# Optimization experiments

Measured on AMD Instinct MI355X. Metric: run time of the kernel, lower is better.

The kernel has to match this reference:

```python
import jax, jax.numpy as jnp
import numpy as np

LATENT, HID, STYLE, D, B = 16, 512, 64, 8, 16384


def _lin(key, fan_in, fan_out):
    kw, kb = jax.random.split(key)
    s = 1.0 / np.sqrt(fan_in)
    return (jax.random.uniform(kw, (fan_in, fan_out), jnp.float32, -s, s),
            jax.random.uniform(kb, (fan_out,), jnp.float32, -s, s))


def setup_inputs() -> dict:
    key = jax.random.key(0)
    ks = jax.random.split(key, 12)
    x = jax.random.normal(ks[0], (B, LATENT), jnp.float32)
    y = jax.random.randint(ks[1], (B,), 0, D)
    # shared MLP: latent->512, 512->512 x3, each followed by ReLU
    W0, b0 = _lin(ks[2], LATENT, HID)
    W1, b1 = _lin(ks[3], HID, HID)
    W2, b2 = _lin(ks[4], HID, HID)
    W3, b3 = _lin(ks[5], HID, HID)
    # unshared per-domain 4-layer MLPs, stacked along domain axis d
    def _stack(k, fi, fo):
        Ws, bs = [], []
        for kk in jax.random.split(k, D):
            w, b = _lin(kk, fi, fo)
            Ws.append(w); bs.append(b)
        return jnp.stack(Ws), jnp.stack(bs)
    U0, c0 = _stack(ks[6], HID, HID)
    U1, c1 = _stack(ks[7], HID, HID)
    U2, c2 = _stack(ks[8], HID, HID)
    U3, c3 = _stack(ks[9], HID, STYLE)
    return {"x": x, "y": y,
            "W0": W0, "b0": b0, "W1": W1, "b1": b1,
            "W2": W2, "b2": b2, "W3": W3, "b3": b3,
            "U0": U0, "c0": c0, "U1": U1, "c1": c1,
            "U2": U2, "c2": c2, "U3": U3, "c3": c3}


def reference(x, y, W0, b0, W1, b1, W2, b2, W3, b3,
              U0, c0, U1, c1, U2, c2, U3, c3):
    # shared trunk
    h = jax.nn.relu(x @ W0 + b0)
    h = jax.nn.relu(h @ W1 + b1)
    h = jax.nn.relu(h @ W2 + b2)
    h = jax.nn.relu(h @ W3 + b3)            # [B, HID]
    # run all D expert MLPs batched, then select per-sample by domain y
    g = jax.nn.relu(jnp.einsum('bi,dio->dbo', h, U0) + c0[:, None, :])
    g = jax.nn.relu(jnp.einsum('dbi,dio->dbo', g, U1) + c1[:, None, :])
    g = jax.nn.relu(jnp.einsum('dbi,dio->dbo', g, U2) + c2[:, None, :])
    g = jnp.einsum('dbi,dio->dbo', g, U3) + c3[:, None, :]   # [D, B, STYLE]
    out = g[y, jnp.arange(g.shape[1])]       # [B, STYLE]
    return out
```

## Files before the change

### kernel.cpp

```cpp
#include <hip/hip_runtime.h>

typedef _Float16 f16;
typedef _Float16 f16x4 __attribute__((ext_vector_type(4)));
typedef _Float16 f16x8 __attribute__((ext_vector_type(8)));
typedef float f32x4 __attribute__((ext_vector_type(4)));

#define B_TOT 16384
#define LAT_  16
#define STY_  64
#define ND_   8

#define ROWS 64
#define NTHR 1024
#define NBLK 256


__global__ void prep_k(const float* W0, f16* Wt0, const float* W1, f16* Wt1,
                       const float* W2, f16* Wt2, const float* W3, f16* Wt3,
                       const float* U0, f16* U0t, const float* U1, f16* U1t,
                       const float* U2, f16* U2t, const float* U3, f16* U3t) {
  int z = blockIdx.z;
  const float* src; f16* dst; int Kin, Nin, Kpad, NR;
  if (z == 0)      { src = W0; dst = Wt0; Kin = 16;  Nin = 512; Kpad = 32;  NR = 512; }
  else if (z == 1) { src = W1; dst = Wt1; Kin = 512; Nin = 512; Kpad = 512; NR = 512; }
  else if (z == 2) { src = W2; dst = Wt2; Kin = 512; Nin = 512; Kpad = 512; NR = 512; }
  else if (z == 3) { src = W3; dst = Wt3; Kin = 512; Nin = 512; Kpad = 512; NR = 512; }
  else if (z < 12) { int d = z - 4;  src = U0 + (long)d * 262144; dst = U0t + (long)d * 262144; Kin = 512; Nin = 512; Kpad = 512; NR = 512; }
  else if (z < 20) { int d = z - 12; src = U1 + (long)d * 262144; dst = U1t + (long)d * 262144; Kin = 512; Nin = 512; Kpad = 512; NR = 512; }
  else if (z < 28) { int d = z - 20; src = U2 + (long)d * 262144; dst = U2t + (long)d * 262144; Kin = 512; Nin = 512; Kpad = 512; NR = 512; }
  else             { int d = z - 28; src = U3 + (long)d * 32768;  dst = U3t + (long)d * 32768;  Kin = 512; Nin = 64;  Kpad = 512; NR = 64; }

  __shared__ float tile[32][33];
  int k0 = blockIdx.y * 32, n0 = blockIdx.x * 32;
  int tx = threadIdx.x, ty = threadIdx.y;
  #pragma unroll
  for (int i = 0; i < 32; i += 8) {
    int k = k0 + ty + i, n = n0 + tx;
    tile[ty + i][tx] = (k < Kin && n < Nin) ? src[(long)k * Nin + n] : 0.f;
  }
  __syncthreads();
  #pragma unroll
  for (int i = 0; i < 32; i += 8) {
    int n = n0 + ty + i, k = k0 + tx;
    if (n < NR && k < Kpad)
      dst[(long)(((k >> 5) * NR + n) << 5) | (k & 31)] = (f16)tile[tx][ty + i];
  }
}

#define NT_BUCKET 1024
#define RPT 16

__global__ __launch_bounds__(NT_BUCKET) void bucket_k(const int* __restrict__ y,
                                                      int* __restrict__ offsets,
                                                      int* __restrict__ perm) {
  __shared__ int hist[ND_][NT_BUCKET];
  __shared__ int totals[ND_];
  __shared__ int bases[ND_ + 1];
  int t = threadIdx.x;
  int base = t * RPT;

  #pragma unroll
  for (int d = 0; d < ND_; d++) hist[d][t] = 0;
  int yv[RPT];
  #pragma unroll
  for (int i = 0; i < RPT; i++) {
    yv[i] = y[base + i];
    hist[yv[i]][t]++;
  }
  __syncthreads();

  int wave = t >> 6, lane = t & 63;
  if (wave < ND_) {
    int d = wave;
    int carry = 0;
    for (int c = 0; c < NT_BUCKET; c += 64) {
      int v = hist[d][c + lane];
      int s = v;
      #pragma unroll
      for (int off = 1; off < 64; off <<= 1) {
        int u = __shfl_up(s, off, 64);
        if (lane >= off) s += u;
      }
      hist[d][c + lane] = carry + s - v;
      carry += __shfl(s, 63, 64);
    }
    if (lane == 0) totals[d] = carry;
  }
  __syncthreads();

  if (t == 0) {
    int s = 0;
    #pragma unroll
    for (int d = 0; d < ND_; d++) { bases[d] = s; offsets[d] = s; s += totals[d]; }
    bases[ND_] = s; offsets[ND_] = s;
  }
  __syncthreads();

  #pragma unroll
  for (int i = 0; i < RPT; i++) {
    int d = yv[i];
    int pos = bases[d] + hist[d][t];
    hist[d][t]++;
    perm[pos] = base + i;
  }
}

#define MFMA_(b, a, c) __builtin_amdgcn_mfma_f32_16x16x32_f16((b), (a), (c), 0, 0, 0)

template<int KT, bool FINAL>
__device__ __forceinline__ void do_layer(
    const f16* __restrict__ Wk, const float* __restrict__ bias,
    f16* __restrict__ act, int rlo, int rhi,
    const int* __restrict__ perm, int slot0, float* __restrict__ out, int t) {
  const int lane = t & 63, wid = t >> 6;
  const int lr = lane & 15, lg = lane >> 4;
  char* actb = (char*)act;

  __syncthreads();

  if (!FINAL) {
    const int wn = wid * 32;
    const f16* wp[2];
    #pragma unroll
    for (int n = 0; n < 2; n++)
      wp[n] = Wk + ((wn + n * 16 + lr) * 32 + lg * 8);
    const char* ab[4];
    #pragma unroll
    for (int m = 0; m < 4; m++)
      ab[m] = actb + m * 1024 + lg * 256 + lr * 16;

    f32x4 acc[4][2];
    #pragma unroll
    for (int m = 0; m < 4; m++) {
      acc[m][0] = f32x4{0.f, 0.f, 0.f, 0.f};
      acc[m][1] = f32x4{0.f, 0.f, 0.f, 0.f};
    }

    f16x8 bf[4][2], af[2][4];
    #pragma unroll
    for (int n = 0; n < 2; n++) bf[0][n] = *(const f16x8*)(wp[n]);
    if constexpr (KT > 1) {
      #pragma unroll
      for (int n = 0; n < 2; n++) bf[1][n] = *(const f16x8*)(wp[n] + 16384);
    }
    if constexpr (KT > 2) {
      #pragma unroll
      for (int n = 0; n < 2; n++) bf[2][n] = *(const f16x8*)(wp[n] + 2 * 16384);
    }
    #pragma unroll
    for (int m = 0; m < 4; m++) af[0][m] = *(const f16x8*)(ab[m]);

    #pragma unroll
    for (int kt = 0; kt < KT; kt++) {
      if (kt + 3 < KT) {
        #pragma unroll
        for (int n = 0; n < 2; n++)
          bf[(kt + 3) & 3][n] = *(const f16x8*)(wp[n] + (kt + 3) * 16384);
      }
      if (kt + 1 < KT) {
        #pragma unroll
        for (int m = 0; m < 4; m++)
          af[(kt + 1) & 1][m] = *(const f16x8*)(ab[m] + (kt + 1) * 4096);
      }
      #pragma unroll
      for (int m = 0; m < 4; m++)
        #pragma unroll
        for (int n = 0; n < 2; n++)
          acc[m][n] = MFMA_(bf[kt & 3][n], af[kt & 1][m], acc[m][n]);
    }

    __syncthreads();

    #pragma unroll
    for (int m = 0; m < 4; m++) {
      int r = m * 16 + lr;
      bool ok = (r >= rlo) && (r < rhi);
      #pragma unroll
      for (int n = 0; n < 2; n++) {
        f32x4 bb = *(const f32x4*)(bias + wn + n * 16 + lg * 4);
        f16x4 h;
        #pragma unroll
        for (int j = 0; j < 4; j++)
          h[j] = (f16)fmaxf(acc[m][n][j] + bb[j], 0.f);
        int byte = (wid * 4 + m) * 1024 + (n * 2 + (lg >> 1)) * 256
                 + lr * 16 + (lg & 1) * 8;
        if (ok)
          *(f16x4*)(actb + byte) = h;
      }
    }
  } else {
    const int mf = wid >> 2, nf = wid & 3;
    const f16* wp = Wk + ((nf * 16 + lr) * 32 + lg * 8);
    const char* abf = actb + mf * 1024 + lg * 256 + lr * 16;
    f32x4 a = f32x4{0.f, 0.f, 0.f, 0.f};
    f16x8 wbuf[4], abuf[2];
    wbuf[0] = *(const f16x8*)(wp);
    wbuf[1] = *(const f16x8*)(wp + 2048);
    wbuf[2] = *(const f16x8*)(wp + 2 * 2048);
    abuf[0] = *(const f16x8*)(abf);
    #pragma unroll
    for (int kt = 0; kt < 16; kt++) {
      if (kt + 3 < 16) wbuf[(kt + 3) & 3] = *(const f16x8*)(wp + (kt + 3) * 2048);
      if (kt + 1 < 16) abuf[(kt + 1) & 1] = *(const f16x8*)(abf + (kt + 1) * 4096);
      a = MFMA_(wbuf[kt & 3], abuf[kt & 1], a);
    }
    int r = mf * 16 + lr;
    if (r >= rlo && r < rhi) {
      int orig = perm[slot0 + r];
      int cn0 = nf * 16 + lg * 4;
      f32x4 bb = *(const f32x4*)(bias + cn0);
      f32x4 v;
      #pragma unroll
      for (int j = 0; j < 4; j++) v[j] = a[j] + bb[j];
      *(f32x4*)(out + (long)orig * STY_ + cn0) = v;
    }
  }
}

__global__ __launch_bounds__(NTHR, 4) void fused_k(
    const float* __restrict__ x,
    const f16* __restrict__ Wt0, const float* __restrict__ b0,
    const f16* __restrict__ Wt1, const float* __restrict__ b1,
    const f16* __restrict__ Wt2, const float* __restrict__ b2,
    const f16* __restrict__ Wt3, const float* __restrict__ b3,
    const f16* __restrict__ U0t, const float* __restrict__ c0,
    const f16* __restrict__ U1t, const float* __restrict__ c1,
    const f16* __restrict__ U2t, const float* __restrict__ c2,
    const f16* __restrict__ U3t, const float* __restrict__ c3,
    const int* __restrict__ offs, const int* __restrict__ perm,
    float* __restrict__ out) {
  __shared__ f16 act[16 * 64 * 32];

  int t = threadIdx.x;
  int wg = (blockIdx.x & 7) * (NBLK / 8) + (blockIdx.x >> 3);
  int slot0 = wg * ROWS;

  char* actb = (char*)act;
  #pragma unroll
  for (int i = 0; i < 2; i++) {
    int e = i * NTHR + t;
    int r = e >> 5, c = e & 31;
    int orig = perm[slot0 + r];
    f16 v = (c < LAT_) ? (f16)x[orig * LAT_ + c] : (f16)0.f;
    int byte = (r >> 4) * 1024 + ((c >> 3) & 3) * 256 + (r & 15) * 16 + (c & 7) * 2;
    *(f16*)(actb + byte) = v;
  }

  int d0 = 0, d1 = 0;
  #pragma unroll
  for (int d = 1; d < ND_; d++) {
    d0 += (slot0 >= offs[d]);
    d1 += (slot0 + ROWS - 1 >= offs[d]);
  }

  do_layer<1,  false>(Wt0, b0, act, 0, ROWS, perm, slot0, out, t);
  do_layer<16, false>(Wt1, b1, act, 0, ROWS, perm, slot0, out, t);
  do_layer<16, false>(Wt2, b2, act, 0, ROWS, perm, slot0, out, t);
  do_layer<16, false>(Wt3, b3, act, 0, ROWS, perm, slot0, out, t);

  #pragma unroll 1
  for (int d = d0; d <= d1; d++) {
    int rlo = (d == d0) ? 0 : (offs[d] - slot0);
    int rhi = (d == d1) ? ROWS : (offs[d + 1] - slot0);
    do_layer<16, false>(U0t + (long)d * 262144, c0 + d * 512,
                        act, rlo, rhi, perm, slot0, out, t);
  }
  #pragma unroll 1
  for (int d = d0; d <= d1; d++) {
    int rlo = (d == d0) ? 0 : (offs[d] - slot0);
    int rhi = (d == d1) ? ROWS : (offs[d + 1] - slot0);
    do_layer<16, false>(U1t + (long)d * 262144, c1 + d * 512,
                        act, rlo, rhi, perm, slot0, out, t);
  }
  #pragma unroll 1
  for (int d = d0; d <= d1; d++) {
    int rlo = (d == d0) ? 0 : (offs[d] - slot0);
    int rhi = (d == d1) ? ROWS : (offs[d + 1] - slot0);
    do_layer<16, false>(U2t + (long)d * 262144, c2 + d * 512,
                        act, rlo, rhi, perm, slot0, out, t);
  }
  #pragma unroll 1
  for (int d = d0; d <= d1; d++) {
    int rlo = (d == d0) ? 0 : (offs[d] - slot0);
    int rhi = (d == d1) ? ROWS : (offs[d + 1] - slot0);
    do_layer<16, true>(U3t + (long)d * 32768, c3 + d * 64,
                       act, rlo, rhi, perm, slot0, out, t);
  }
}


extern "C" void kernel_launch(void* const* d_in, const int* in_sizes, int n_in,
                              void* d_out, int out_size, void* d_ws, size_t ws_size,
                              hipStream_t stream) {
  const float* x  = (const float*)d_in[0];
  const int*   y  = (const int*)  d_in[1];
  const float* W0 = (const float*)d_in[2];
  const float* b0 = (const float*)d_in[3];
  const float* W1 = (const float*)d_in[4];
  const float* b1 = (const float*)d_in[5];
  const float* W2 = (const float*)d_in[6];
  const float* b2 = (const float*)d_in[7];
  const float* W3 = (const float*)d_in[8];
  const float* b3 = (const float*)d_in[9];
  const float* U0 = (const float*)d_in[10];
  const float* c0 = (const float*)d_in[11];
  const float* U1 = (const float*)d_in[12];
  const float* c1 = (const float*)d_in[13];
  const float* U2 = (const float*)d_in[14];
  const float* c2 = (const float*)d_in[15];
  const float* U3 = (const float*)d_in[16];
  const float* c3 = (const float*)d_in[17];
  float* out = (float*)d_out;

  char* p = (char*)d_ws;
  auto alloc = [&](size_t bytes) -> char* {
    char* r = p; p += (bytes + 255) & ~(size_t)255; return r;
  };
  f16* Wt0 = (f16*)alloc((size_t)512 * 32 * 2);
  f16* Wt1 = (f16*)alloc((size_t)512 * 512 * 2);
  f16* Wt2 = (f16*)alloc((size_t)512 * 512 * 2);
  f16* Wt3 = (f16*)alloc((size_t)512 * 512 * 2);
  f16* U0t = (f16*)alloc((size_t)ND_ * 512 * 512 * 2);
  f16* U1t = (f16*)alloc((size_t)ND_ * 512 * 512 * 2);
  f16* U2t = (f16*)alloc((size_t)ND_ * 512 * 512 * 2);
  f16* U3t = (f16*)alloc((size_t)ND_ * 16 * 64 * 32 * 2);
  int* offsets = (int*)alloc((ND_ + 1) * 4);
  int* perm    = (int*)alloc((size_t)B_TOT * 4);

  prep_k<<<dim3(16, 16, 36), dim3(32, 8), 0, stream>>>(W0, Wt0, W1, Wt1, W2, Wt2, W3, Wt3,
                                                       U0, U0t, U1, U1t, U2, U2t, U3, U3t);
  bucket_k<<<1, NT_BUCKET, 0, stream>>>(y, offsets, perm);
  fused_k<<<NBLK, NTHR, 0, stream>>>(x, Wt0, b0, Wt1, b1, Wt2, b2, Wt3, b3,
                                     U0t, c0, U1t, c1, U2t, c2, U3t, c3,
                                     offsets, perm, out);
}
```

Baseline: 113.9 us.

## Merge weight prep, bucketing and fused MLP into one cooperative kernel

```diff
diff --git a/kernel.cpp b/kernel.cpp
--- a/kernel.cpp
+++ b/kernel.cpp
@@ -1,4 +1,7 @@
 #include <hip/hip_runtime.h>
+#include <hip/hip_cooperative_groups.h>
+
+namespace cg = cooperative_groups;
 
 typedef _Float16 f16;
 typedef _Float16 f16x4 __attribute__((ext_vector_type(4)));
@@ -14,96 +17,8 @@
 #define NTHR 1024
 #define NBLK 256
 
-
-__global__ void prep_k(const float* W0, f16* Wt0, const float* W1, f16* Wt1,
-                       const float* W2, f16* Wt2, const float* W3, f16* Wt3,
-                       const float* U0, f16* U0t, const float* U1, f16* U1t,
-                       const float* U2, f16* U2t, const float* U3, f16* U3t) {
-  int z = blockIdx.z;
-  const float* src; f16* dst; int Kin, Nin, Kpad, NR;
-  if (z == 0)      { src = W0; dst = Wt0; Kin = 16;  Nin = 512; Kpad = 32;  NR = 512; }
-  else if (z == 1) { src = W1; dst = Wt1; Kin = 512; Nin = 512; Kpad = 512; NR = 512; }
-  else if (z == 2) { src = W2; dst = Wt2; Kin = 512; Nin = 512; Kpad = 512; NR = 512; }
-  else if (z == 3) { src = W3; dst = Wt3; Kin = 512; Nin = 512; Kpad = 512; NR = 512; }
-  else if (z < 12) { int d = z - 4;  src = U0 + (long)d * 262144; dst = U0t + (long)d * 262144; Kin = 512; Nin = 512; Kpad = 512; NR = 512; }
-  else if (z < 20) { int d = z - 12; src = U1 + (long)d * 262144; dst = U1t + (long)d * 262144; Kin = 512; Nin = 512; Kpad = 512; NR = 512; }
-  else if (z < 28) { int d = z - 20; src = U2 + (long)d * 262144; dst = U2t + (long)d * 262144; Kin = 512; Nin = 512; Kpad = 512; NR = 512; }
-  else             { int d = z - 28; src = U3 + (long)d * 32768;  dst = U3t + (long)d * 32768;  Kin = 512; Nin = 64;  Kpad = 512; NR = 64; }
-
-  __shared__ float tile[32][33];
-  int k0 = blockIdx.y * 32, n0 = blockIdx.x * 32;
-  int tx = threadIdx.x, ty = threadIdx.y;
-  #pragma unroll
-  for (int i = 0; i < 32; i += 8) {
-    int k = k0 + ty + i, n = n0 + tx;
-    tile[ty + i][tx] = (k < Kin && n < Nin) ? src[(long)k * Nin + n] : 0.f;
-  }
-  __syncthreads();
-  #pragma unroll
-  for (int i = 0; i < 32; i += 8) {
-    int n = n0 + ty + i, k = k0 + tx;
-    if (n < NR && k < Kpad)
-      dst[(long)(((k >> 5) * NR + n) << 5) | (k & 31)] = (f16)tile[tx][ty + i];
-  }
-}
-
-#define NT_BUCKET 1024
-#define RPT 16
-
-__global__ __launch_bounds__(NT_BUCKET) void bucket_k(const int* __restrict__ y,
-                                                      int* __restrict__ offsets,
-                                                      int* __restrict__ perm) {
-  __shared__ int hist[ND_][NT_BUCKET];
-  __shared__ int totals[ND_];
-  __shared__ int bases[ND_ + 1];
-  int t = threadIdx.x;
-  int base = t * RPT;
-
-  #pragma unroll
-  for (int d = 0; d < ND_; d++) hist[d][t] = 0;
-  int yv[RPT];
-  #pragma unroll
-  for (int i = 0; i < RPT; i++) {
-    yv[i] = y[base + i];
-    hist[yv[i]][t]++;
-  }
-  __syncthreads();
-
-  int wave = t >> 6, lane = t & 63;
-  if (wave < ND_) {
-    int d = wave;
-    int carry = 0;
-    for (int c = 0; c < NT_BUCKET; c += 64) {
-      int v = hist[d][c + lane];
-      int s = v;
-      #pragma unroll
-      for (int off = 1; off < 64; off <<= 1) {
-        int u = __shfl_up(s, off, 64);
-        if (lane >= off) s += u;
-      }
-      hist[d][c + lane] = carry + s - v;
-      carry += __shfl(s, 63, 64);
-    }
-    if (lane == 0) totals[d] = carry;
-  }
-  __syncthreads();
-
-  if (t == 0) {
-    int s = 0;
-    #pragma unroll
-    for (int d = 0; d < ND_; d++) { bases[d] = s; offsets[d] = s; s += totals[d]; }
-    bases[ND_] = s; offsets[ND_] = s;
-  }
-  __syncthreads();
-
-  #pragma unroll
-  for (int i = 0; i < RPT; i++) {
-    int d = yv[i];
-    int pos = bases[d] + hist[d][t];
-    hist[d][t]++;
-    perm[pos] = base + i;
-  }
-}
+#define NTILE 7184
+
 
 #define MFMA_(b, a, c) __builtin_amdgcn_mfma_f32_16x16x32_f16((b), (a), (c), 0, 0, 0)
 
@@ -118,7 +33,7 @@
 
   __syncthreads();
 
-  if (!FINAL) {
+  if constexpr (!FINAL) {
     const int wn = wid * 32;
     const f16* wp[2];
     #pragma unroll
@@ -217,25 +132,118 @@
   }
 }
 
-__global__ __launch_bounds__(NTHR, 4) void fused_k(
-    const float* __restrict__ x,
-    const f16* __restrict__ Wt0, const float* __restrict__ b0,
-    const f16* __restrict__ Wt1, const float* __restrict__ b1,
-    const f16* __restrict__ Wt2, const float* __restrict__ b2,
-    const f16* __restrict__ Wt3, const float* __restrict__ b3,
-    const f16* __restrict__ U0t, const float* __restrict__ c0,
-    const f16* __restrict__ U1t, const float* __restrict__ c1,
-    const f16* __restrict__ U2t, const float* __restrict__ c2,
-    const f16* __restrict__ U3t, const float* __restrict__ c3,
-    const int* __restrict__ offs, const int* __restrict__ perm,
+__global__ __launch_bounds__(NTHR, 4) void mega_k(
+    const float* __restrict__ x, const int* __restrict__ y,
+    const float* W0, const float* b0, const float* W1, const float* b1,
+    const float* W2, const float* b2, const float* W3, const float* b3,
+    const float* U0, const float* c0, const float* U1, const float* c1,
+    const float* U2, const float* c2, const float* U3, const float* c3,
+    f16* Wt0, f16* Wt1, f16* Wt2, f16* Wt3,
+    f16* U0t, f16* U1t, f16* U2t, f16* U3t,
+    int* __restrict__ offsets, int* __restrict__ perm,
     float* __restrict__ out) {
-  __shared__ f16 act[16 * 64 * 32];
+  __shared__ __align__(16) char smem[65536];
 
   int t = threadIdx.x;
-  int wg = (blockIdx.x & 7) * (NBLK / 8) + (blockIdx.x >> 3);
+  int bid = blockIdx.x;
+
+  if (bid < 255) {
+    float (*tile)[32][33] = (float (*)[32][33])smem;
+    int sub = t >> 8, tt = t & 255;
+    int tx = tt & 31, ty = tt >> 5;
+    for (int it = 0; it < 8; ++it) {
+      int g = (it * 255 + bid) * 4 + sub;
+      bool active = (g < NTILE);
+      int gg = active ? g : 0;
+      int z, nx, ky;
+      if (gg < 16)        { z = 0; nx = gg; ky = 0; }
+      else if (gg < 6928) { int r = gg - 16; z = 1 + (r >> 8); r &= 255; ky = r >> 4; nx = r & 15; }
+      else                { int r = gg - 6928; z = 28 + (r >> 5); r &= 31; nx = r >> 4; ky = r & 15; }
+      const float* src; f16* dst; int Kin, Nin, Kpad, NR;
+      if (z == 0)      { src = W0; dst = Wt0; Kin = 16;  Nin = 512; Kpad = 32;  NR = 512; }
+      else if (z == 1) { src = W1; dst = Wt1; Kin = 512; Nin = 512; Kpad = 512; NR = 512; }
+      else if (z == 2) { src = W2; dst = Wt2; Kin = 512; Nin = 512; Kpad = 512; NR = 512; }
+      else if (z == 3) { src = W3; dst = Wt3; Kin = 512; Nin = 512; Kpad = 512; NR = 512; }
+      else if (z < 12) { int d = z - 4;  src = U0 + (long)d * 262144; dst = U0t + (long)d * 262144; Kin = 512; Nin = 512; Kpad = 512; NR = 512; }
+      else if (z < 20) { int d = z - 12; src = U1 + (long)d * 262144; dst = U1t + (long)d * 262144; Kin = 512; Nin = 512; Kpad = 512; NR = 512; }
+      else if (z < 28) { int d = z - 20; src = U2 + (long)d * 262144; dst = U2t + (long)d * 262144; Kin = 512; Nin = 512; Kpad = 512; NR = 512; }
+      else             { int d = z - 28; src = U3 + (long)d * 32768;  dst = U3t + (long)d * 32768;  Kin = 512; Nin = 64;  Kpad = 512; NR = 64; }
+
+      int k0 = ky * 32, n0 = nx * 32;
+      #pragma unroll
+      for (int i = 0; i < 32; i += 8) {
+        int k = k0 + ty + i, n = n0 + tx;
+        tile[sub][ty + i][tx] =
+            (active && k < Kin && n < Nin) ? src[(long)k * Nin + n] : 0.f;
+      }
+      __syncthreads();
+      #pragma unroll
+      for (int i = 0; i < 32; i += 8) {
+        int n = n0 + ty + i, k = k0 + tx;
+        if (active && n < NR && k < Kpad)
+          dst[(long)(((k >> 5) * NR + n) << 5) | (k & 31)] = (f16)tile[sub][tx][ty + i];
+      }
+      __syncthreads();
+    }
+  } else {
+    int (*hist)[NTHR] = (int (*)[NTHR])smem;
+    __shared__ int totals[ND_];
+    __shared__ int bases[ND_];
+    #pragma unroll
+    for (int d = 0; d < ND_; d++) hist[d][t] = 0;
+    int base = t * 16;
+    int yv[16];
+    #pragma unroll
+    for (int i = 0; i < 16; i++) {
+      yv[i] = y[base + i];
+      hist[yv[i]][t]++;
+    }
+    __syncthreads();
+
+    int wave = t >> 6, lane = t & 63;
+    if (wave < ND_) {
+      int d = wave;
+      int carry = 0;
+      for (int c = 0; c < NTHR; c += 64) {
+        int v = hist[d][c + lane];
+        int s = v;
+        #pragma unroll
+        for (int off = 1; off < 64; off <<= 1) {
+          int u = __shfl_up(s, off, 64);
+          if (lane >= off) s += u;
+        }
+        hist[d][c + lane] = carry + s - v;
+        carry += __shfl(s, 63, 64);
+      }
+      if (lane == 0) totals[d] = carry;
+    }
+    __syncthreads();
+
+    if (t == 0) {
+      int s = 0;
+      #pragma unroll
+      for (int d = 0; d < ND_; d++) { bases[d] = s; offsets[d] = s; s += totals[d]; }
+      offsets[ND_] = s;
+    }
+    __syncthreads();
+
+    #pragma unroll
+    for (int i = 0; i < 16; i++) {
+      int d = yv[i];
+      int pos = bases[d] + hist[d][t];
+      hist[d][t]++;
+      perm[pos] = base + i;
+    }
+  }
+
+  cg::this_grid().sync();
+
+  f16* act = (f16*)smem;
+  char* actb = smem;
+
+  int wg = (bid & 7) * (NBLK / 8) + (bid >> 3);
   int slot0 = wg * ROWS;
 
-  char* actb = (char*)act;
   #pragma unroll
   for (int i = 0; i < 2; i++) {
     int e = i * NTHR + t;
@@ -249,8 +257,8 @@
   int d0 = 0, d1 = 0;
   #pragma unroll
   for (int d = 1; d < ND_; d++) {
-    d0 += (slot0 >= offs[d]);
-    d1 += (slot0 + ROWS - 1 >= offs[d]);
+    d0 += (slot0 >= offsets[d]);
+    d1 += (slot0 + ROWS - 1 >= offsets[d]);
   }
 
   do_layer<1,  false>(Wt0, b0, act, 0, ROWS, perm, slot0, out, t);
@@ -260,29 +268,29 @@
 
   #pragma unroll 1
   for (int d = d0; d <= d1; d++) {
-    int rlo = (d == d0) ? 0 : (offs[d] - slot0);
-    int rhi = (d == d1) ? ROWS : (offs[d + 1] - slot0);
+    int rlo = (d == d0) ? 0 : (offsets[d] - slot0);
+    int rhi = (d == d1) ? ROWS : (offsets[d + 1] - slot0);
     do_layer<16, false>(U0t + (long)d * 262144, c0 + d * 512,
                         act, rlo, rhi, perm, slot0, out, t);
   }
   #pragma unroll 1
   for (int d = d0; d <= d1; d++) {
-    int rlo = (d == d0) ? 0 : (offs[d] - slot0);
-    int rhi = (d == d1) ? ROWS : (offs[d + 1] - slot0);
+    int rlo = (d == d0) ? 0 : (offsets[d] - slot0);
+    int rhi = (d == d1) ? ROWS : (offsets[d + 1] - slot0);
     do_layer<16, false>(U1t + (long)d * 262144, c1 + d * 512,
                         act, rlo, rhi, perm, slot0, out, t);
   }
   #pragma unroll 1
   for (int d = d0; d <= d1; d++) {
-    int rlo = (d == d0) ? 0 : (offs[d] - slot0);
-    int rhi = (d == d1) ? ROWS : (offs[d + 1] - slot0);
+    int rlo = (d == d0) ? 0 : (offsets[d] - slot0);
+    int rhi = (d == d1) ? ROWS : (offsets[d + 1] - slot0);
     do_layer<16, false>(U2t + (long)d * 262144, c2 + d * 512,
                         act, rlo, rhi, perm, slot0, out, t);
   }
   #pragma unroll 1
   for (int d = d0; d <= d1; d++) {
-    int rlo = (d == d0) ? 0 : (offs[d] - slot0);
-    int rhi = (d == d1) ? ROWS : (offs[d + 1] - slot0);
+    int rlo = (d == d0) ? 0 : (offsets[d] - slot0);
+    int rhi = (d == d1) ? ROWS : (offsets[d + 1] - slot0);
     do_layer<16, true>(U3t + (long)d * 32768, c3 + d * 64,
                        act, rlo, rhi, perm, slot0, out, t);
   }
@@ -327,10 +335,16 @@
   int* offsets = (int*)alloc((ND_ + 1) * 4);
   int* perm    = (int*)alloc((size_t)B_TOT * 4);
 
-  prep_k<<<dim3(16, 16, 36), dim3(32, 8), 0, stream>>>(W0, Wt0, W1, Wt1, W2, Wt2, W3, Wt3,
-                                                       U0, U0t, U1, U1t, U2, U2t, U3, U3t);
-  bucket_k<<<1, NT_BUCKET, 0, stream>>>(y, offsets, perm);
-  fused_k<<<NBLK, NTHR, 0, stream>>>(x, Wt0, b0, Wt1, b1, Wt2, b2, Wt3, b3,
-                                     U0t, c0, U1t, c1, U2t, c2, U3t, c3,
-                                     offsets, perm, out);
+  void* args[] = {
+    (void*)&x, (void*)&y,
+    (void*)&W0, (void*)&b0, (void*)&W1, (void*)&b1,
+    (void*)&W2, (void*)&b2, (void*)&W3, (void*)&b3,
+    (void*)&U0, (void*)&c0, (void*)&U1, (void*)&c1,
+    (void*)&U2, (void*)&c2, (void*)&U3, (void*)&c3,
+    (void*)&Wt0, (void*)&Wt1, (void*)&Wt2, (void*)&Wt3,
+    (void*)&U0t, (void*)&U1t, (void*)&U2t, (void*)&U3t,
+    (void*)&offsets, (void*)&perm, (void*)&out
+  };
+  hipLaunchCooperativeKernel((const void*)mega_k, dim3(NBLK), dim3(NTHR),
+                             args, 0, stream);
 }
```

Result: slower. 142.7 us (+25.3%).

## Stage weight tiles into LDS via direct global-to-LDS loads with double buffering

Applied to the files above, without the earlier changes.

```diff
diff --git a/kernel.cpp b/kernel.cpp
--- a/kernel.cpp
+++ b/kernel.cpp
@@ -14,6 +14,12 @@
 #define NTHR 1024
 #define NBLK 256
 
+
+__device__ __forceinline__ void gload16(const f16* g, f16* l) {
+  __builtin_amdgcn_global_load_lds(
+      (const __attribute__((address_space(1))) unsigned int*)g,
+      (__attribute__((address_space(3))) unsigned int*)l, 16, 0, 0);
+}
 
 __global__ void prep_k(const float* W0, f16* Wt0, const float* W1, f16* Wt1,
                        const float* W2, f16* Wt2, const float* W3, f16* Wt3,
@@ -42,8 +48,11 @@
   #pragma unroll
   for (int i = 0; i < 32; i += 8) {
     int n = n0 + ty + i, k = k0 + tx;
-    if (n < NR && k < Kpad)
-      dst[(long)(((k >> 5) * NR + n) << 5) | (k & 31)] = (f16)tile[tx][ty + i];
+    if (n < NR && k < Kpad) {
+      long idx = (long)(k >> 5) * (NR * 32) + (n >> 4) * 512
+               + ((k >> 3) & 3) * 128 + (n & 15) * 8 + (k & 7);
+      dst[idx] = (f16)tile[tx][ty + i];
+    }
   }
 }
 
@@ -92,7 +101,7 @@
     int s = 0;
     #pragma unroll
     for (int d = 0; d < ND_; d++) { bases[d] = s; offsets[d] = s; s += totals[d]; }
-    bases[ND_] = s; offsets[ND_] = s;
+    offsets[ND_] = s;
   }
   __syncthreads();
 
@@ -110,20 +119,16 @@
 template<int KT, bool FINAL>
 __device__ __forceinline__ void do_layer(
     const f16* __restrict__ Wk, const float* __restrict__ bias,
-    f16* __restrict__ act, int rlo, int rhi,
+    f16* __restrict__ act, f16* __restrict__ wls,
+    int rlo, int rhi,
     const int* __restrict__ perm, int slot0, float* __restrict__ out, int t) {
   const int lane = t & 63, wid = t >> 6;
   const int lr = lane & 15, lg = lane >> 4;
   char* actb = (char*)act;
 
-  __syncthreads();
-
-  if (!FINAL) {
+  if constexpr (!FINAL) {
     const int wn = wid * 32;
-    const f16* wp[2];
-    #pragma unroll
-    for (int n = 0; n < 2; n++)
-      wp[n] = Wk + ((wn + n * 16 + lr) * 32 + lg * 8);
+    const f16* wsrc = Wk + wid * 512 + lane * 8;
     const char* ab[4];
     #pragma unroll
     for (int m = 0; m < 4; m++)
@@ -136,40 +141,32 @@
       acc[m][1] = f32x4{0.f, 0.f, 0.f, 0.f};
     }
 
-    f16x8 bf[4][2], af[2][4];
-    #pragma unroll
-    for (int n = 0; n < 2; n++) bf[0][n] = *(const f16x8*)(wp[n]);
-    if constexpr (KT > 1) {
-      #pragma unroll
-      for (int n = 0; n < 2; n++) bf[1][n] = *(const f16x8*)(wp[n] + 16384);
-    }
-    if constexpr (KT > 2) {
-      #pragma unroll
-      for (int n = 0; n < 2; n++) bf[2][n] = *(const f16x8*)(wp[n] + 2 * 16384);
-    }
-    #pragma unroll
-    for (int m = 0; m < 4; m++) af[0][m] = *(const f16x8*)(ab[m]);
+    gload16(wsrc, wls + wid * 512);
+    gload16(wsrc + 8192, wls + 8192 + wid * 512);
+    __syncthreads();
 
     #pragma unroll
     for (int kt = 0; kt < KT; kt++) {
-      if (kt + 3 < KT) {
-        #pragma unroll
-        for (int n = 0; n < 2; n++)
-          bf[(kt + 3) & 3][n] = *(const f16x8*)(wp[n] + (kt + 3) * 16384);
+      if (kt + 1 < KT) {
+        const f16* s = wsrc + (kt + 1) * 16384;
+        f16* d = wls + ((kt + 1) & 1) * 16384;
+        gload16(s, d + wid * 512);
+        gload16(s + 8192, d + 8192 + wid * 512);
       }
-      if (kt + 1 < KT) {
-        #pragma unroll
-        for (int m = 0; m < 4; m++)
-          af[(kt + 1) & 1][m] = *(const f16x8*)(ab[m] + (kt + 1) * 4096);
+      const f16* wb = wls + (kt & 1) * 16384;
+      f16x8 b0 = *(const f16x8*)(wb + (wid * 2 + 0) * 512 + lane * 8);
+      f16x8 b1 = *(const f16x8*)(wb + (wid * 2 + 1) * 512 + lane * 8);
+      f16x8 af[4];
+      #pragma unroll
+      for (int m = 0; m < 4; m++)
+        af[m] = *(const f16x8*)(ab[m] + kt * 4096);
+      #pragma unroll
+      for (int m = 0; m < 4; m++) {
+        acc[m][0] = MFMA_(b0, af[m], acc[m][0]);
+        acc[m][1] = MFMA_(b1, af[m], acc[m][1]);
       }
-      #pragma unroll
-      for (int m = 0; m < 4; m++)
-        #pragma unroll
-        for (int n = 0; n < 2; n++)
-          acc[m][n] = MFMA_(bf[kt & 3][n], af[kt & 1][m], acc[m][n]);
-    }
-
-    __syncthreads();
+      __syncthreads();
+    }
 
     #pragma unroll
     for (int m = 0; m < 4; m++) {
@@ -189,8 +186,9 @@
       }
     }
   } else {
+    __syncthreads();
     const int mf = wid >> 2, nf = wid & 3;
-    const f16* wp = Wk + ((nf * 16 + lr) * 32 + lg * 8);
+    const f16* wp = Wk + nf * 512 + lg * 128 + lr * 8;
     const char* abf = actb + mf * 1024 + lg * 256 + lr * 16;
     f32x4 a = f32x4{0.f, 0.f, 0.f, 0.f};
     f16x8 wbuf[4], abuf[2];
@@ -230,6 +228,7 @@
     const int* __restrict__ offs, const int* __restrict__ perm,
     float* __restrict__ out) {
   __shared__ f16 act[16 * 64 * 32];
+  __shared__ f16 wls[2][16384];
 
   int t = threadIdx.x;
   int wg = (blockIdx.x & 7) * (NBLK / 8) + (blockIdx.x >> 3);
@@ -253,38 +252,38 @@
     d1 += (slot0 + ROWS - 1 >= offs[d]);
   }
 
-  do_layer<1,  false>(Wt0, b0, act, 0, ROWS, perm, slot0, out, t);
-  do_layer<16, false>(Wt1, b1, act, 0, ROWS, perm, slot0, out, t);
-  do_layer<16, false>(Wt2, b2, act, 0, ROWS, perm, slot0, out, t);
-  do_layer<16, false>(Wt3, b3, act, 0, ROWS, perm, slot0, out, t);
+  do_layer<1,  false>(Wt0, b0, act, &wls[0][0], 0, ROWS, perm, slot0, out, t);
+  do_layer<16, false>(Wt1, b1, act, &wls[0][0], 0, ROWS, perm, slot0, out, t);
+  do_layer<16, false>(Wt2, b2, act, &wls[0][0], 0, ROWS, perm, slot0, out, t);
+  do_layer<16, false>(Wt3, b3, act, &wls[0][0], 0, ROWS, perm, slot0, out, t);
 
   #pragma unroll 1
   for (int d = d0; d <= d1; d++) {
     int rlo = (d == d0) ? 0 : (offs[d] - slot0);
     int rhi = (d == d1) ? ROWS : (offs[d + 1] - slot0);
     do_layer<16, false>(U0t + (long)d * 262144, c0 + d * 512,
-                        act, rlo, rhi, perm, slot0, out, t);
+                        act, &wls[0][0], rlo, rhi, perm, slot0, out, t);
   }
   #pragma unroll 1
   for (int d = d0; d <= d1; d++) {
     int rlo = (d == d0) ? 0 : (offs[d] - slot0);
     int rhi = (d == d1) ? ROWS : (offs[d + 1] - slot0);
     do_layer<16, false>(U1t + (long)d * 262144, c1 + d * 512,
-                        act, rlo, rhi, perm, slot0, out, t);
+                        act, &wls[0][0], rlo, rhi, perm, slot0, out, t);
   }
   #pragma unroll 1
   for (int d = d0; d <= d1; d++) {
     int rlo = (d == d0) ? 0 : (offs[d] - slot0);
     int rhi = (d == d1) ? ROWS : (offs[d + 1] - slot0);
     do_layer<16, false>(U2t + (long)d * 262144, c2 + d * 512,
-                        act, rlo, rhi, perm, slot0, out, t);
+                        act, &wls[0][0], rlo, rhi, perm, slot0, out, t);
   }
   #pragma unroll 1
   for (int d = d0; d <= d1; d++) {
     int rlo = (d == d0) ? 0 : (offs[d] - slot0);
     int rhi = (d == d1) ? ROWS : (offs[d + 1] - slot0);
     do_layer<16, true>(U3t + (long)d * 32768, c3 + d * 64,
-                       act, rlo, rhi, perm, slot0, out, t);
+                       act, &wls[0][0], rlo, rhi, perm, slot0, out, t);
   }
 }
 
```

Result: slower. 128.5 us (+12.9%).
